# Optimization experiments

Measured on AMD Instinct MI355X. Metric: run time of the kernel, lower is better.

Reference implementation:

```python
import jax, jax.numpy as jnp
import numpy as np

HID, HEADS, NL, WIN = 512, 4, 2, 5
DH = HID // HEADS
SLOPE = 0.2
EPS = 1e-5
B, L = 16, 1024
NEG_INF = -1e30


def _layer_norm(x, g, b):
    m = jnp.mean(x, axis=-1, keepdims=True)
    v = jnp.mean(jnp.square(x - m), axis=-1, keepdims=True)
    return (x - m) * jax.lax.rsqrt(v + EPS) * g + b


def _build_masks(attention_mask, last_starts, seq_len):
    # node layout: [g, h_1..h_T, l], total N = seq_len + 2
    bsz = attention_mask.shape[0]
    N = seq_len + 2
    pos = jnp.arange(N)
    last = last_starts[:, None, None]  # (B,1,1)
    global_mask = jnp.ones((bsz, 1, N), jnp.float32)
    # local node: g, itself, and tokens of the last utterance (node idx last+1 .. seq_len)
    local_mask = ((pos == 0) | (pos == N - 1) | ((pos >= last + 1) & (pos <= seq_len))).astype(jnp.float32)  # (B,1,N)
    # token nodes: global node + window of neighboring tokens
    ii = jnp.arange(seq_len)[:, None]          # query token index
    jj = jnp.arange(N)[None, :]                # key node index
    t = jj - 1                                 # token index of key node (valid in [0, seq_len))
    win = (t >= 0) & (t < seq_len) & (jnp.abs(ii - t) <= WIN)
    base = (jj == 0) | win                     # (L,N)
    # tokens at/after last utterance start also attend to the local node
    to_local = (jnp.arange(seq_len)[None, :, None] >= last_starts[:, None, None]) & (jj[None] == N - 1)  # (B,L,N)
    token_mask = (base[None] | to_local).astype(jnp.float32)
    # padding: key tokens masked by attention_mask; g and l always visible; padded queries fully masked
    ones_col = jnp.ones((bsz, seq_len, 1), jnp.float32)
    pad = jnp.concatenate([ones_col, jnp.broadcast_to(attention_mask[:, None, :], (bsz, seq_len, seq_len)), ones_col], axis=-1)
    token_mask = token_mask * pad * attention_mask[:, :, None]
    return global_mask, local_mask, token_mask


def _gat(q, kv, W, a, mask):
    # W: (hid, hid) as torch Linear weight (out,in); a: (H, 2*DH)
    bsz, Lq, _ = q.shape
    N = kv.shape[1]
    Q = (q @ W.T).reshape(bsz, Lq, HEADS, DH)
    K = (kv @ W.T).reshape(bsz, N, HEADS, DH)
    V = K  # key==value tensor in this module, same projection
    # additive score decomposes: (a . [Q||K]) = Q.a_q + K.a_k
    sq = jnp.einsum('bqhd,hd->bhq', Q, a[:, :DH])
    sk = jnp.einsum('bkhd,hd->bhk', K, a[:, DH:])
    s = sq[:, :, :, None] + sk[:, :, None, :]           # (B,H,Lq,N)
    s = jnp.where(s >= 0, s, SLOPE * s)                 # LeakyReLU
    s = jnp.where(mask[:, None, :, :] > 0, s, NEG_INF)
    w = jax.nn.softmax(s, axis=-1)
    w = jnp.where(jnp.isnan(w), 0.0, w)
    out = jnp.einsum('bhqk,bkhd->bqhd', w, V)
    return out.reshape(bsz, Lq, HID)


def setup_inputs() -> dict:
    key = jax.random.key(0)
    ks = jax.random.split(key, 10)
    scale = 1.0 / np.sqrt(HID)
    return {
        'global_embedding': jax.random.normal(ks[0], (B, HID), jnp.float32),
        'token_embeddings': jax.random.normal(ks[1], (B, L, HID), jnp.float32),
        'local_embedding': jax.random.normal(ks[2], (B, HID), jnp.float32),
        'attention_mask': jnp.ones((B, L), jnp.float32),
        'last_utterance_starts': jax.random.randint(ks[3], (B,), 0, 512, jnp.int32),
        'gat_W': jax.random.normal(ks[4], (NL, HID, HID), jnp.float32) * scale,
        'gat_a': jax.random.normal(ks[5], (NL, HEADS, 2 * DH), jnp.float32) * scale,
        'ln_gamma': jnp.ones((NL, HID), jnp.float32),
        'ln_beta': jnp.zeros((NL, HID), jnp.float32),
        'ffn_w1': jax.random.normal(ks[6], (3, HID, 4 * HID), jnp.float32) * scale,
        'ffn_b1': jnp.zeros((3, 4 * HID), jnp.float32),
        'ffn_w2': jax.random.normal(ks[7], (3, 4 * HID, HID), jnp.float32) * (1.0 / np.sqrt(4 * HID)),
        'ffn_b2': jnp.zeros((3, HID), jnp.float32),
        'out_ln_gamma': jnp.ones((3, HID), jnp.float32),
        'out_ln_beta': jnp.zeros((3, HID), jnp.float32),
    }


def reference(global_embedding, token_embeddings, local_embedding, attention_mask,
              last_utterance_starts, gat_W, gat_a, ln_gamma, ln_beta,
              ffn_w1, ffn_b1, ffn_w2, ffn_b2, out_ln_gamma, out_ln_beta):
    bsz, seq_len, _ = token_embeddings.shape
    gm, lm, tm = _build_masks(attention_mask, last_utterance_starts, seq_len)
    g = global_embedding[:, None, :]
    h = token_embeddings
    l = local_embedding[:, None, :]
    nodes = jnp.concatenate([g, h, l], axis=1)
    for k in range(NL):
        g_new = jax.nn.elu(_gat(g, nodes, gat_W[k], gat_a[k], gm))
        h_new = jax.nn.elu(_gat(h, nodes, gat_W[k], gat_a[k], tm))
        l_new = jax.nn.elu(_gat(l, nodes, gat_W[k], gat_a[k], lm))
        g = _layer_norm(g + g_new, ln_gamma[k], ln_beta[k])
        h = _layer_norm(h + h_new, ln_gamma[k], ln_beta[k])
        l = _layer_norm(l + l_new, ln_gamma[k], ln_beta[k])
        nodes = jnp.concatenate([g, h, l], axis=1)
    def ffn(x, i):
        hmid = jax.nn.gelu(x @ ffn_w1[i] + ffn_b1[i], approximate=False)
        return hmid @ ffn_w2[i] + ffn_b2[i]
    g = g + ffn(g, 0)
    h = h + ffn(h, 1)
    l = l + ffn(l, 2)
    updated_global = _layer_norm(g[:, 0], out_ln_gamma[0], out_ln_beta[0])
    updated_tokens = _layer_norm(h, out_ln_gamma[1], out_ln_beta[1])
    updated_local = _layer_norm(l[:, 0], out_ln_gamma[2], out_ln_beta[2])
    return updated_global, updated_tokens, updated_local
```

## Files before the change

kernel.cpp:

```cpp
#include <hip/hip_runtime.h>
#include <stdint.h>
#include <math.h>

#define HIDN 512
#define NHEAD 4
#define DHEAD 128
#define BATCH 16
#define SEQ 1024
#define NNODE 1026
#define MROWS (BATCH * NNODE)
#define MPAD 16512
#define MTOK (BATCH * SEQ)
#define FFD 2048
#define JCH 114

typedef short bf16x8 __attribute__((ext_vector_type(8)));
typedef float f32x4 __attribute__((ext_vector_type(4)));

__device__ __forceinline__ float bf2f(ushort u) {
    union { uint32_t i; float f; } v; v.i = ((uint32_t)u) << 16; return v.f;
}
__device__ __forceinline__ ushort f2bf(float f) {
    uint32_t x = __float_as_uint(f);
    return (ushort)((x + 0x7fffu + ((x >> 16) & 1u)) >> 16);
}
__device__ __forceinline__ float gelu(float v) {
    return 0.5f * v * (1.f + erff(v * 0.70710678118654752f));
}
__device__ __forceinline__ int cswz(int row, int col) {
    return row * 128 + ((((col >> 2) ^ (row & 7)) & 31) << 2) + (col & 3);
}

__global__ __launch_bounds__(256) void k_build_nodes(
    const float* __restrict__ g, const float* __restrict__ tok,
    const float* __restrict__ l, ushort* __restrict__ nb)
{
    int idx = blockIdx.x * 256 + threadIdx.x;
    int r = idx >> 9, c = idx & 511;
    float u = 0.f;
    if (r < MROWS) {
        int b = r / NNODE;
        int n = r - b * NNODE;
        if (n == 0)            u = g[b * HIDN + c];
        else if (n <= SEQ)     u = tok[((size_t)b * SEQ + (n - 1)) * HIDN + c];
        else                   u = l[b * HIDN + c];
    }
    nb[idx] = f2bf(u);
}

__global__ __launch_bounds__(256) void k_cvt(
    const float* __restrict__ in, ushort* __restrict__ out, int n)
{
    int idx = blockIdx.x * 256 + threadIdx.x;
    if (idx < n) out[idx] = f2bf(in[idx]);
}

__global__ __launch_bounds__(256) void k_transpose(
    const float* __restrict__ in, ushort* __restrict__ out, int R, int C)
{
    __shared__ float t[32][33];
    int x = blockIdx.x * 32 + threadIdx.x;
    int y0 = blockIdx.y * 32;
    for (int dy = threadIdx.y; dy < 32; dy += 8)
        t[dy][threadIdx.x] = in[(size_t)(y0 + dy) * C + x];
    __syncthreads();
    int ox = y0 + threadIdx.x;
    int oy0 = blockIdx.x * 32;
    for (int dy = threadIdx.y; dy < 32; dy += 8)
        out[(size_t)(oy0 + dy) * R + ox] = f2bf(t[threadIdx.x][dy]);
}

#define BM 128
#define BN 128
#define BK 64

__global__ __launch_bounds__(256) void k_gemm_bt(
    const ushort* __restrict__ A, const ushort* __restrict__ Bt,
    float* __restrict__ Cf, ushort* __restrict__ Cb,
    const float* __restrict__ bias,
    int N, int K, int ldb, int mode, int amap, int mguard, int first)
{
    __shared__ ushort smem[BM * BK + BN * BK];
    ushort* sA = smem;
    ushort* sB = smem + BM * BK;
    int tid = threadIdx.x;
    int lane = tid & 63;
    int wave = tid >> 6;
    int wm = wave >> 1, wn = wave & 1;
    int m0 = blockIdx.y * BM;
    int n0 = blockIdx.x * BN;

    f32x4 acc[4][4];
#pragma unroll
    for (int i = 0; i < 4; ++i)
#pragma unroll
        for (int j = 0; j < 4; ++j) acc[i][j] = (f32x4){0.f, 0.f, 0.f, 0.f};

    int lr = lane >> 3;
    int gco = ((lane & 7) ^ lr) * 8;

    for (int k0 = 0; k0 < K; k0 += BK) {
#pragma unroll
        for (int t = 0; t < 4; ++t) {
            int q = wave * 4 + t;
            int rr8 = q * 8 + lr;
            int grA = m0 + rr8;
            if (amap) grA = grA + 2 * (grA >> 10) + 1;
            const ushort* gpA = A + (size_t)grA * K + (k0 + gco);
            __builtin_amdgcn_global_load_lds(
                (const __attribute__((address_space(1))) void*)gpA,
                (__attribute__((address_space(3))) void*)&sA[q * 512], 16, 0, 0);
            int grB = n0 + rr8;
            const ushort* gpB = Bt + (size_t)grB * ldb + (k0 + gco);
            __builtin_amdgcn_global_load_lds(
                (const __attribute__((address_space(1))) void*)gpB,
                (__attribute__((address_space(3))) void*)&sB[q * 512], 16, 0, 0);
        }
        __syncthreads();
        int rr = lane & 7;
        int rhi = (lane & 15) >> 3;
#pragma unroll
        for (int kk = 0; kk < BK; kk += 32) {
            int c4 = (kk >> 3) + (lane >> 4);
            int swz = rr * 64 + ((c4 ^ rr) << 3);
            bf16x8 af[4], bfr[4];
#pragma unroll
            for (int i = 0; i < 4; ++i)
                af[i] = *reinterpret_cast<const bf16x8*>(&sA[(wm * 8 + i * 2 + rhi) * 512 + swz]);
#pragma unroll
            for (int j = 0; j < 4; ++j)
                bfr[j] = *reinterpret_cast<const bf16x8*>(&sB[(wn * 8 + j * 2 + rhi) * 512 + swz]);
#pragma unroll
            for (int i = 0; i < 4; ++i)
#pragma unroll
                for (int j = 0; j < 4; ++j)
                    acc[i][j] = __builtin_amdgcn_mfma_f32_16x16x32_bf16(af[i], bfr[j], acc[i][j], 0, 0, 0);
        }
        __syncthreads();
    }

    float* sC = (float*)smem;
    int rb = (lane >> 4) * 4;
    int cb = lane & 15;
    int lrow = tid >> 2;
    int lcol = (tid & 3) << 5;
#pragma unroll
    for (int pass = 0; pass < 2; ++pass) {
        if (wm == pass) {
#pragma unroll
            for (int i = 0; i < 4; ++i)
#pragma unroll
                for (int j = 0; j < 4; ++j)
#pragma unroll
                    for (int rg = 0; rg < 4; ++rg)
                        sC[cswz(i * 16 + rb + rg, wn * 64 + j * 16 + cb)] = acc[i][j][rg];
        }
        __syncthreads();
        int gm = m0 + pass * 64 + lrow;
        if (gm < mguard) {
            int gn0 = n0 + lcol;
            float v[32];
#pragma unroll
            for (int e4 = 0; e4 < 8; ++e4) {
                float4 t = *(const float4*)&sC[cswz(lrow, lcol + e4 * 4)];
                v[e4 * 4 + 0] = t.x; v[e4 * 4 + 1] = t.y;
                v[e4 * 4 + 2] = t.z; v[e4 * 4 + 3] = t.w;
            }
            if (mode == 1 || mode == 3) {
                uint4* dst = (uint4*)(Cb + (size_t)gm * N + gn0);
#pragma unroll
                for (int q2 = 0; q2 < 4; ++q2) {
                    float s[8];
#pragma unroll
                    for (int t = 0; t < 8; ++t) {
                        float x = v[q2 * 8 + t];
                        s[t] = (mode == 1) ? gelu(x + bias[gn0 + q2 * 8 + t]) : x;
                    }
                    uint4 w;
                    w.x = (uint32_t)f2bf(s[0]) | ((uint32_t)f2bf(s[1]) << 16);
                    w.y = (uint32_t)f2bf(s[2]) | ((uint32_t)f2bf(s[3]) << 16);
                    w.z = (uint32_t)f2bf(s[4]) | ((uint32_t)f2bf(s[5]) << 16);
                    w.w = (uint32_t)f2bf(s[6]) | ((uint32_t)f2bf(s[7]) << 16);
                    dst[q2] = w;
                }
            } else {
                float4* dst = (float4*)(Cf + (size_t)gm * N + gn0);
#pragma unroll
                for (int e4 = 0; e4 < 8; ++e4) {
                    float4 t;
                    t.x = v[e4 * 4 + 0]; t.y = v[e4 * 4 + 1];
                    t.z = v[e4 * 4 + 2]; t.w = v[e4 * 4 + 3];
                    if (!first) {
                        float4 o = dst[e4];
                        t.x += o.x; t.y += o.y; t.z += o.z; t.w += o.w;
                    }
                    dst[e4] = t;
                }
            }
        }
        __syncthreads();
    }
}

__global__ __launch_bounds__(256) void k_sqsk(
    const ushort* __restrict__ P, const float* __restrict__ a,
    float* __restrict__ sq, float* __restrict__ sk)
{
    int wave = threadIdx.x >> 6, lane = threadIdx.x & 63;
    int row = blockIdx.x * 4 + wave;
    if (row >= MROWS) return;
    int hh = lane >> 4;
    int o0 = lane * 8;
    int dl = o0 & 127;
    const ushort* p = P + (size_t)row * HIDN + o0;
    const float* a1 = a + hh * 256 + dl;
    const float* a2 = a1 + 128;
    float s1 = 0.f, s2 = 0.f;
#pragma unroll
    for (int d = 0; d < 8; ++d) {
        float pv = bf2f(p[d]);
        s1 += pv * a1[d];
        s2 += pv * a2[d];
    }
#pragma unroll
    for (int off = 8; off; off >>= 1) {
        s1 += __shfl_xor(s1, off);
        s2 += __shfl_xor(s2, off);
    }
    if ((lane & 15) == 0) {
        sq[row * 4 + hh] = s1;
        sk[row * 4 + hh] = s2;
    }
}

__global__ __launch_bounds__(64) void k_attn_token(
    const ushort* __restrict__ P, const float* __restrict__ sq, const float* __restrict__ sk,
    const float* __restrict__ am, const int* __restrict__ last,
    const float* __restrict__ gam, const float* __restrict__ bet,
    ushort* __restrict__ nb)
{
    int bid = blockIdx.x;
    int tokid = ((bid & 7) << 11) | (bid >> 3);
    int b = tokid >> 10, i = tokid & 1023;
    int lane = threadIdx.x;
    int hh = lane >> 4;
    int base = b * NNODE;
    int qrow = base + 1 + i;

    int kr[13];
    int val[13];
    int rowok = am[b * SEQ + i] > 0.f ? 1 : 0;
    kr[0] = base; val[0] = rowok;
#pragma unroll
    for (int s = 0; s < 11; ++s) {
        int t = i - 5 + s;
        int inb = (t >= 0) && (t <= SEQ - 1);
        int tt = inb ? t : 0;
        int v = inb && rowok && (am[b * SEQ + tt] > 0.f);
        kr[1 + s] = base + 1 + tt;
        val[1 + s] = v;
    }
    kr[12] = base + SEQ + 1;
    val[12] = (rowok && (i >= last[b])) ? 1 : 0;

    float sqv = sq[qrow * 4 + hh];
    float sc[13];
    float mx = -1e30f;
#pragma unroll
    for (int t = 0; t < 13; ++t) {
        float s = 0.f;
        if (val[t]) {
            s = sqv + sk[kr[t] * 4 + hh];
            s = s >= 0.f ? s : 0.2f * s;
            mx = fmaxf(mx, s);
        }
        sc[t] = s;
    }
    float den = 0.f;
#pragma unroll
    for (int t = 0; t < 13; ++t) {
        float ev = 0.f;
        if (val[t]) ev = expf(sc[t] - mx);
        sc[t] = ev; den += ev;
    }
    float inv = (den > 1e-30f && den < 1e30f) ? 1.f / den : 0.f;

    int o0 = lane * 8;
    float accv[8] = {0.f, 0.f, 0.f, 0.f, 0.f, 0.f, 0.f, 0.f};
#pragma unroll
    for (int t = 0; t < 13; ++t) {
        if (val[t]) {
            float wgt = sc[t] * inv;
            const ushort* pv = P + (size_t)kr[t] * HIDN + o0;
#pragma unroll
            for (int d = 0; d < 8; ++d) accv[d] += wgt * bf2f(pv[d]);
        }
    }

    ushort* nrow = nb + (size_t)qrow * HIDN + o0;
    float x[8], s1 = 0.f, s2 = 0.f;
#pragma unroll
    for (int d = 0; d < 8; ++d) {
        float v = accv[d];
        v = v > 0.f ? v : expf(v) - 1.f;
        v += bf2f(nrow[d]);
        x[d] = v; s1 += v; s2 += v * v;
    }
#pragma unroll
    for (int off = 32; off; off >>= 1) { s1 += __shfl_xor(s1, off); s2 += __shfl_xor(s2, off); }
    float mean = s1 * (1.f / 512.f);
    float var = s2 * (1.f / 512.f) - mean * mean; var = fmaxf(var, 0.f);
    float rn = rsqrtf(var + 1e-5f);
#pragma unroll
    for (int d = 0; d < 8; ++d) {
        float y = (x[d] - mean) * rn * gam[o0 + d] + bet[o0 + d];
        nrow[d] = f2bf(y);
    }
}

__global__ __launch_bounds__(256) void k_glsm(
    const float* __restrict__ sq, const float* __restrict__ sk,
    const int* __restrict__ last,
    float* __restrict__ ebuf, float* __restrict__ einv)
{
    __shared__ float red[1024];
    int rw = blockIdx.x, b = rw >> 1, isl = rw & 1;
    int base = b * NNODE;
    int qrow = base + (isl ? (SEQ + 1) : 0);
    int lastb = last[b];
    int tid = threadIdx.x;

    float sqh[4];
#pragma unroll
    for (int h = 0; h < 4; ++h) sqh[h] = sq[qrow * 4 + h];

    float mx[4] = {-1e30f, -1e30f, -1e30f, -1e30f};
    for (int j = tid; j < NNODE; j += 256) {
        bool ok = !isl || (j == 0 || j == SEQ + 1 || (j >= lastb + 1 && j <= SEQ));
        if (ok) {
#pragma unroll
            for (int h = 0; h < 4; ++h) {
                float s = sqh[h] + sk[(base + j) * 4 + h];
                s = s >= 0.f ? s : 0.2f * s;
                mx[h] = fmaxf(mx[h], s);
            }
        }
    }
#pragma unroll
    for (int h = 0; h < 4; ++h) red[tid * 4 + h] = mx[h];
    __syncthreads();
    for (int s = 128; s; s >>= 1) {
        if (tid < s) {
#pragma unroll
            for (int h = 0; h < 4; ++h)
                red[tid * 4 + h] = fmaxf(red[tid * 4 + h], red[(tid + s) * 4 + h]);
        }
        __syncthreads();
    }
#pragma unroll
    for (int h = 0; h < 4; ++h) mx[h] = red[h];
    __syncthreads();

    float sm[4] = {0.f, 0.f, 0.f, 0.f};
    for (int j = tid; j < NNODE; j += 256) {
        bool ok = !isl || (j == 0 || j == SEQ + 1 || (j >= lastb + 1 && j <= SEQ));
#pragma unroll
        for (int h = 0; h < 4; ++h) {
            float v = 0.f;
            if (ok) {
                float s = sqh[h] + sk[(base + j) * 4 + h];
                s = s >= 0.f ? s : 0.2f * s;
                v = expf(s - mx[h]);
            }
            ebuf[((size_t)rw * NNODE + j) * 4 + h] = v;
            sm[h] += v;
        }
    }
#pragma unroll
    for (int h = 0; h < 4; ++h) red[tid * 4 + h] = sm[h];
    __syncthreads();
    for (int s = 128; s; s >>= 1) {
        if (tid < s) {
#pragma unroll
            for (int h = 0; h < 4; ++h) red[tid * 4 + h] += red[(tid + s) * 4 + h];
        }
        __syncthreads();
    }
    if (tid < 4) {
        float den = red[tid];
        einv[rw * 4 + tid] = (den > 1e-30f && den < 1e30f) ? 1.f / den : 0.f;
    }
}

__global__ __launch_bounds__(256) void k_glpv(
    const ushort* __restrict__ P, const float* __restrict__ ebuf,
    float* __restrict__ pout2)
{
    __shared__ float es[JCH * 4];
    int p = blockIdx.x, rw = blockIdx.y;
    int b = rw >> 1;
    int base = b * NNODE;
    int tid = threadIdx.x;
    for (int t = tid; t < JCH * 4; t += 256)
        es[t] = ebuf[((size_t)rw * NNODE + p * JCH) * 4 + t];
    __syncthreads();
    int o0 = tid, o1 = tid + 256;
    int h0 = o0 >> 7, h1 = o1 >> 7;
    const ushort* Pb = P + (size_t)(base + p * JCH) * HIDN;
    float a0 = 0.f, a1 = 0.f;
    for (int j = 0; j < JCH; ++j) {
        const ushort* pr = Pb + (size_t)j * HIDN;
        a0 += es[j * 4 + h0] * bf2f(pr[o0]);
        a1 += es[j * 4 + h1] * bf2f(pr[o1]);
    }
    float* o = pout2 + ((size_t)rw * 9 + p) * HIDN;
    o[o0] = a0;
    o[o1] = a1;
}

__global__ __launch_bounds__(256) void k_glred(
    const float* __restrict__ pout2, const float* __restrict__ einv,
    const float* __restrict__ gam, const float* __restrict__ bet,
    ushort* __restrict__ nb)
{
    __shared__ float red[512];
    int rw = blockIdx.x, b = rw >> 1, isl = rw & 1;
    size_t qrow = (size_t)b * NNODE + (isl ? SEQ + 1 : 0);
    int tid = threadIdx.x;
    float xv[2], s1 = 0.f, s2 = 0.f;
#pragma unroll
    for (int u = 0; u < 2; ++u) {
        int o = tid + u * 256;
        int h = o >> 7;
        float acc = 0.f;
#pragma unroll
        for (int p = 0; p < 9; ++p)
            acc += pout2[((size_t)rw * 9 + p) * HIDN + o];
        acc *= einv[rw * 4 + h];
        float v = acc > 0.f ? acc : expf(acc) - 1.f;
        v += bf2f(nb[qrow * HIDN + o]);
        xv[u] = v; s1 += v; s2 += v * v;
    }
    red[tid] = s1;
    __syncthreads();
    for (int s = 128; s; s >>= 1) { if (tid < s) red[tid] += red[tid + s]; __syncthreads(); }
    float mean = red[0] * (1.f / 512.f);
    __syncthreads();
    red[tid] = s2;
    __syncthreads();
    for (int s = 128; s; s >>= 1) { if (tid < s) red[tid] += red[tid + s]; __syncthreads(); }
    float var = red[0] * (1.f / 512.f) - mean * mean; var = fmaxf(var, 0.f);
    float rn = rsqrtf(var + 1e-5f);
#pragma unroll
    for (int u = 0; u < 2; ++u) {
        int o = tid + u * 256;
        float y = (xv[u] - mean) * rn * gam[o] + bet[o];
        nb[qrow * HIDN + o] = f2bf(y);
    }
}

__global__ __launch_bounds__(256) void k_fgl1(
    const ushort* __restrict__ nb, const float* __restrict__ w1,
    float* __restrict__ pmid)
{
    __shared__ float xs[64];
    int p = blockIdx.x, rw = blockIdx.y;
    int b = rw >> 1, isl = rw & 1;
    int idx = isl ? 2 : 0;
    size_t nrow = (size_t)b * NNODE + (isl ? SEQ + 1 : 0);
    int tid = threadIdx.x;
    if (tid < 64) xs[tid] = bf2f(nb[nrow * HIDN + p * 64 + tid]);
    __syncthreads();
    const float* W1 = w1 + (size_t)idx * HIDN * FFD + (size_t)p * 64 * FFD;
    float acc[8] = {0.f, 0.f, 0.f, 0.f, 0.f, 0.f, 0.f, 0.f};
    for (int ii = 0; ii < 64; ++ii) {
        float xv = xs[ii];
        const float* wrow = W1 + (size_t)ii * FFD + tid;
#pragma unroll
        for (int u = 0; u < 8; ++u) acc[u] += xv * wrow[u * 256];
    }
    float* o = pmid + ((size_t)rw * 8 + p) * FFD + tid;
#pragma unroll
    for (int u = 0; u < 8; ++u) o[u * 256] = acc[u];
}

__global__ __launch_bounds__(256) void k_fgl2(
    const float* __restrict__ pmid, const float* __restrict__ b1,
    float* __restrict__ mid)
{
    int g = blockIdx.x * 256 + threadIdx.x;
    int e4 = g * 4;
    int rw = e4 >> 11;
    int m = e4 & 2047;
    int isl = rw & 1;
    int idx = isl ? 2 : 0;
#pragma unroll
    for (int d = 0; d < 4; ++d) {
        float s = 0.f;
#pragma unroll
        for (int p = 0; p < 8; ++p)
            s += pmid[((size_t)rw * 8 + p) * FFD + m + d];
        s += b1[idx * FFD + m + d];
        mid[(size_t)rw * FFD + m + d] = gelu(s);
    }
}

__global__ __launch_bounds__(256) void k_fgl3(
    const float* __restrict__ mid, const float* __restrict__ w2,
    float* __restrict__ pout)
{
    __shared__ float ms[256];
    int p = blockIdx.x, rw = blockIdx.y;
    int isl = rw & 1;
    int idx = isl ? 2 : 0;
    int tid = threadIdx.x;
    ms[tid] = mid[(size_t)rw * FFD + p * 256 + tid];
    __syncthreads();
    const float* W2 = w2 + (size_t)idx * FFD * HIDN + (size_t)p * 256 * HIDN;
    float a0 = 0.f, a1 = 0.f;
    for (int mm = 0; mm < 256; ++mm) {
        float mv = ms[mm];
        const float* wrow = W2 + (size_t)mm * HIDN + tid;
        a0 += mv * wrow[0];
        a1 += mv * wrow[256];
    }
    float* o = pout + ((size_t)rw * 8 + p) * HIDN + tid;
    o[0] = a0;
    o[256] = a1;
}

__global__ __launch_bounds__(256) void k_fgl4(
    const float* __restrict__ pout, const float* __restrict__ b2,
    const ushort* __restrict__ nb,
    const float* __restrict__ og, const float* __restrict__ obt,
    float* __restrict__ out)
{
    __shared__ float red[512];
    int rw = blockIdx.x;
    int b = rw >> 1, isl = rw & 1;
    int idx = isl ? 2 : 0;
    size_t nrow = (size_t)b * NNODE + (isl ? SEQ + 1 : 0);
    int tid = threadIdx.x;
    float xv[2], s1 = 0.f, s2 = 0.f;
#pragma unroll
    for (int u = 0; u < 2; ++u) {
        int o = tid + u * 256;
        float s = 0.f;
#pragma unroll
        for (int p = 0; p < 8; ++p)
            s += pout[((size_t)rw * 8 + p) * HIDN + o];
        s += b2[idx * HIDN + o] + bf2f(nb[nrow * HIDN + o]);
        xv[u] = s; s1 += s; s2 += s * s;
    }
    red[tid] = s1;
    __syncthreads();
    for (int s = 128; s; s >>= 1) { if (tid < s) red[tid] += red[tid + s]; __syncthreads(); }
    float mean = red[0] * (1.f / 512.f);
    __syncthreads();
    red[tid] = s2;
    __syncthreads();
    for (int s = 128; s; s >>= 1) { if (tid < s) red[tid] += red[tid + s]; __syncthreads(); }
    float var = red[0] * (1.f / 512.f) - mean * mean; var = fmaxf(var, 0.f);
    float rn = rsqrtf(var + 1e-5f);
    size_t obase = isl ? ((size_t)8192 + (size_t)MTOK * HIDN + (size_t)b * HIDN)
                       : ((size_t)b * HIDN);
#pragma unroll
    for (int u = 0; u < 2; ++u) {
        int o = tid + u * 256;
        out[obase + o] = (xv[u] - mean) * rn * og[idx * HIDN + o] + obt[idx * HIDN + o];
    }
}

__global__ __launch_bounds__(64) void k_ln_final(
    float* __restrict__ Pt, const ushort* __restrict__ nb,
    const float* __restrict__ b2,
    const float* __restrict__ gam, const float* __restrict__ bet)
{
    int r = blockIdx.x, lane = threadIdx.x;
    int nrow = r + 2 * (r >> 10) + 1;
    int o0 = lane * 8;
    float* x = Pt + (size_t)r * HIDN + o0;
    const ushort* res = nb + (size_t)nrow * HIDN + o0;
    float v[8], s1 = 0.f, s2 = 0.f;
#pragma unroll
    for (int d = 0; d < 8; ++d) {
        float t = x[d] + b2[o0 + d] + bf2f(res[d]);
        v[d] = t; s1 += t; s2 += t * t;
    }
#pragma unroll
    for (int off = 32; off; off >>= 1) { s1 += __shfl_xor(s1, off); s2 += __shfl_xor(s2, off); }
    float mean = s1 * (1.f / 512.f);
    float var = s2 * (1.f / 512.f) - mean * mean; var = fmaxf(var, 0.f);
    float rn = rsqrtf(var + 1e-5f);
#pragma unroll
    for (int d = 0; d < 8; ++d)
        x[d] = (v[d] - mean) * rn * gam[o0 + d] + bet[o0 + d];
}

extern "C" void kernel_launch(void* const* d_in, const int* in_sizes, int n_in,
                              void* d_out, int out_size, void* d_ws, size_t ws_size,
                              hipStream_t stream)
{
    (void)in_sizes; (void)n_in; (void)out_size; (void)ws_size;
    const float* g_emb   = (const float*)d_in[0];
    const float* tok_emb = (const float*)d_in[1];
    const float* l_emb   = (const float*)d_in[2];
    const float* am      = (const float*)d_in[3];
    const int*   last    = (const int*)d_in[4];
    const float* gat_W   = (const float*)d_in[5];
    const float* gat_a   = (const float*)d_in[6];
    const float* ln_g    = (const float*)d_in[7];
    const float* ln_b    = (const float*)d_in[8];
    const float* ffn_w1  = (const float*)d_in[9];
    const float* ffn_b1  = (const float*)d_in[10];
    const float* ffn_w2  = (const float*)d_in[11];
    const float* ffn_b2  = (const float*)d_in[12];
    const float* oln_g   = (const float*)d_in[13];
    const float* oln_b   = (const float*)d_in[14];
    float* out = (float*)d_out;

    char* w = (char*)d_ws;
    ushort* nodes_b = (ushort*)w; w += (size_t)MPAD * HIDN * 2;
    char*   scratch = w;          w += (size_t)8 * 1024 * 1024;
    ushort* w1t     = (ushort*)w; w += (size_t)FFD * HIDN * 2;
    ushort* w2t     = (ushort*)w; w += (size_t)FFD * HIDN * 2;
    ushort* gatWb   = (ushort*)w; w += (size_t)2 * HIDN * HIDN * 2;
    float*  sqb     = (float*)w;  w += (size_t)MPAD * 4 * 4;
    float*  skb     = (float*)w;  w += (size_t)MPAD * 4 * 4;
    ushort* Hmid    = (ushort*)w; w += (size_t)MTOK * FFD * 2;

    float* pmid = (float*)scratch;
    float* mid  = pmid + (size_t)32 * 8 * FFD;
    float* pout = mid + (size_t)32 * FFD;
    float* ebuf  = (float*)(scratch + (size_t)3 * 1024 * 1024);
    float* einv  = ebuf + (size_t)32 * NNODE * 4;
    float* pout2 = einv + 128;

    ushort* P = (ushort*)out;
    float* Pt = out + 8192;

    k_build_nodes<<<MPAD * HIDN / 256, 256, 0, stream>>>(g_emb, tok_emb, l_emb, nodes_b);
    k_cvt<<<(2 * HIDN * HIDN) / 256, 256, 0, stream>>>(gat_W, gatWb, 2 * HIDN * HIDN);
    k_transpose<<<dim3(FFD / 32, HIDN / 32), dim3(32, 8), 0, stream>>>(ffn_w1 + (size_t)HIDN * FFD, w1t, HIDN, FFD);
    k_transpose<<<dim3(HIDN / 32, FFD / 32), dim3(32, 8), 0, stream>>>(ffn_w2 + (size_t)FFD * HIDN, w2t, FFD, HIDN);

    for (int k = 0; k < 2; ++k) {
        k_gemm_bt<<<dim3(HIDN / BN, MPAD / BM), 256, 0, stream>>>(
            nodes_b, gatWb + (size_t)k * HIDN * HIDN, nullptr, P, nullptr,
            HIDN, HIDN, HIDN, 3, 0, MROWS, 1);
        k_sqsk<<<MROWS / 4, 256, 0, stream>>>(P, gat_a + k * NHEAD * 2 * DHEAD, sqb, skb);
        k_attn_token<<<MTOK, 64, 0, stream>>>(P, sqb, skb, am, last,
                                              ln_g + k * HIDN, ln_b + k * HIDN, nodes_b);
        k_glsm<<<32, 256, 0, stream>>>(sqb, skb, last, ebuf, einv);
        k_glpv<<<dim3(9, 32), 256, 0, stream>>>(P, ebuf, pout2);
        k_glred<<<32, 256, 0, stream>>>(pout2, einv, ln_g + k * HIDN, ln_b + k * HIDN, nodes_b);
    }

    k_fgl1<<<dim3(8, 32), 256, 0, stream>>>(nodes_b, ffn_w1, pmid);
    k_fgl2<<<64, 256, 0, stream>>>(pmid, ffn_b1, mid);
    k_fgl3<<<dim3(8, 32), 256, 0, stream>>>(mid, ffn_w2, pout);
    k_fgl4<<<32, 256, 0, stream>>>(pout, ffn_b2, nodes_b, oln_g, oln_b, out);

    k_gemm_bt<<<dim3(FFD / BN, MTOK / BM), 256, 0, stream>>>(
        nodes_b, w1t, nullptr, Hmid,
        ffn_b1 + FFD, FFD, HIDN, HIDN, 1, 1, MTOK, 1);
    k_gemm_bt<<<dim3(HIDN / BN, MTOK / BM), 256, 0, stream>>>(
        Hmid, w2t, Pt, nullptr, nullptr,
        HIDN, FFD, FFD, 0, 0, MTOK, 1);
    k_ln_final<<<MTOK, 64, 0, stream>>>(Pt, nodes_b, ffn_b2 + HIDN, oln_g + HIDN, oln_b + HIDN);
}
```

Before: 536.9 us.

## Double-buffer GEMM LDS tiles and remap workgroups across XCDs

The bf16 GEMM kernel now keeps two LDS stages. The global-to-LDS load for the next K tile is issued before the MFMAs on the current tile, so each iteration ends with a single vmcnt wait plus barrier instead of two barriers. Block IDs are also remapped so that consecutive tiles land on the same XCD, which is meant to improve L2 reuse across the eight chiplets. LDS use doubles to 64KB per block, which may reduce occupancy.

New measurement: 515.3 us. 4.0% less time.

```diff
diff --git a/kernel.cpp b/kernel.cpp
--- a/kernel.cpp
+++ b/kernel.cpp
@@ -80,15 +80,21 @@
     const float* __restrict__ bias,
     int N, int K, int ldb, int mode, int amap, int mguard, int first)
 {
-    __shared__ ushort smem[BM * BK + BN * BK];
-    ushort* sA = smem;
-    ushort* sB = smem + BM * BK;
+    __shared__ ushort smem[2 * (BM * BK + BN * BK)];
     int tid = threadIdx.x;
     int lane = tid & 63;
     int wave = tid >> 6;
     int wm = wave >> 1, wn = wave & 1;
-    int m0 = blockIdx.y * BM;
-    int n0 = blockIdx.x * BN;
+
+    int GX = gridDim.x;
+    int nwg = GX * gridDim.y;
+    int bid = blockIdx.y * GX + blockIdx.x;
+    int q = nwg >> 3, r = nwg & 7;
+    int xcd = bid & 7, pos = bid >> 3;
+    int cbase = (xcd < r) ? xcd * (q + 1) : r * (q + 1) + (xcd - r) * q;
+    int wk = cbase + pos;
+    int m0 = (wk / GX) * BM;
+    int n0 = (wk % GX) * BN;
 
     f32x4 acc[4][4];
 #pragma unroll
@@ -99,26 +105,38 @@
     int lr = lane >> 3;
     int gco = ((lane & 7) ^ lr) * 8;
 
-    for (int k0 = 0; k0 < K; k0 += BK) {
-#pragma unroll
-        for (int t = 0; t < 4; ++t) {
-            int q = wave * 4 + t;
-            int rr8 = q * 8 + lr;
+    auto stage = [&](int buf, int k0) {
+        ushort* sA = smem + buf * (BM * BK + BN * BK);
+        ushort* sB = sA + BM * BK;
+#pragma unroll
+        for (int u = 0; u < 4; ++u) {
+            int qq = wave * 4 + u;
+            int rr8 = qq * 8 + lr;
             int grA = m0 + rr8;
             if (amap) grA = grA + 2 * (grA >> 10) + 1;
             const ushort* gpA = A + (size_t)grA * K + (k0 + gco);
             __builtin_amdgcn_global_load_lds(
                 (const __attribute__((address_space(1))) void*)gpA,
-                (__attribute__((address_space(3))) void*)&sA[q * 512], 16, 0, 0);
+                (__attribute__((address_space(3))) void*)&sA[qq * 512], 16, 0, 0);
             int grB = n0 + rr8;
             const ushort* gpB = Bt + (size_t)grB * ldb + (k0 + gco);
             __builtin_amdgcn_global_load_lds(
                 (const __attribute__((address_space(1))) void*)gpB,
-                (__attribute__((address_space(3))) void*)&sB[q * 512], 16, 0, 0);
-        }
-        __syncthreads();
-        int rr = lane & 7;
-        int rhi = (lane & 15) >> 3;
+                (__attribute__((address_space(3))) void*)&sB[qq * 512], 16, 0, 0);
+        }
+    };
+
+    const int nk = K / BK;
+    stage(0, 0);
+    __syncthreads();
+
+    int rr = lane & 7;
+    int rhi = (lane & 15) >> 3;
+    for (int t = 0; t < nk; ++t) {
+        if (t + 1 < nk) stage((t + 1) & 1, (t + 1) * BK);
+
+        const ushort* sAr = smem + (t & 1) * (BM * BK + BN * BK);
+        const ushort* sBr = sAr + BM * BK;
 #pragma unroll
         for (int kk = 0; kk < BK; kk += 32) {
             int c4 = (kk >> 3) + (lane >> 4);
@@ -126,18 +144,20 @@
             bf16x8 af[4], bfr[4];
 #pragma unroll
             for (int i = 0; i < 4; ++i)
-                af[i] = *reinterpret_cast<const bf16x8*>(&sA[(wm * 8 + i * 2 + rhi) * 512 + swz]);
+                af[i] = *reinterpret_cast<const bf16x8*>(&sAr[(wm * 8 + i * 2 + rhi) * 512 + swz]);
 #pragma unroll
             for (int j = 0; j < 4; ++j)
-                bfr[j] = *reinterpret_cast<const bf16x8*>(&sB[(wn * 8 + j * 2 + rhi) * 512 + swz]);
+                bfr[j] = *reinterpret_cast<const bf16x8*>(&sBr[(wn * 8 + j * 2 + rhi) * 512 + swz]);
 #pragma unroll
             for (int i = 0; i < 4; ++i)
 #pragma unroll
                 for (int j = 0; j < 4; ++j)
                     acc[i][j] = __builtin_amdgcn_mfma_f32_16x16x32_bf16(af[i], bfr[j], acc[i][j], 0, 0, 0);
         }
-        __syncthreads();
-    }
+        asm volatile("s_waitcnt vmcnt(0)" ::: "memory");
+        __builtin_amdgcn_s_barrier();
+    }
+    __syncthreads();
 
     float* sC = (float*)smem;
     int rb = (lane >> 4) * 4;
```
